# Performance work log

Measured on AMD Instinct MI355X. Metric: run time of the kernel, lower is better.

The kernel has to match this reference:

```python
import jax, jax.numpy as jnp
import numpy as np

N, E, H = 100000, 3200000, 128


def setup_inputs() -> dict:
    key = jax.random.key(0)
    ks = jax.random.split(key, 12)
    s = 1.0 / np.sqrt(H)
    x = jax.random.normal(ks[0], (N, H), dtype=jnp.float32)
    edge_index = jax.random.randint(ks[1], (2, E), 0, N, dtype=jnp.int64)
    # GatedGraphConv weight: [num_layers=1, H, H] -> single [H, H]
    W = jax.random.normal(ks[2], (H, H), dtype=jnp.float32) * s
    # GRUCell (gate order: r, z, n)
    gru_w_ih = jax.random.normal(ks[3], (3 * H, H), dtype=jnp.float32) * s
    gru_w_hh = jax.random.normal(ks[4], (3 * H, H), dtype=jnp.float32) * s
    gru_b_ih = jax.random.normal(ks[5], (3 * H,), dtype=jnp.float32) * s
    gru_b_hh = jax.random.normal(ks[6], (3 * H,), dtype=jnp.float32) * s
    # LSTM layer 0 (gate order: i, f, g, o)
    lstm_w_ih = jax.random.normal(ks[7], (4 * H, H), dtype=jnp.float32) * s
    lstm_w_hh = jax.random.normal(ks[8], (4 * H, H), dtype=jnp.float32) * s
    lstm_b_ih = jax.random.normal(ks[9], (4 * H,), dtype=jnp.float32) * s
    lstm_b_hh = jax.random.normal(ks[10], (4 * H,), dtype=jnp.float32) * s
    return {
        "x": x, "edge_index": edge_index, "W": W,
        "gru_w_ih": gru_w_ih, "gru_w_hh": gru_w_hh,
        "gru_b_ih": gru_b_ih, "gru_b_hh": gru_b_hh,
        "lstm_w_ih": lstm_w_ih, "lstm_w_hh": lstm_w_hh,
        "lstm_b_ih": lstm_b_ih, "lstm_b_hh": lstm_b_hh,
    }


def _forward(x, edge_index, W, gru_w_ih, gru_w_hh, gru_b_ih, gru_b_hh,
             lstm_w_ih, lstm_w_hh, lstm_b_ih, lstm_b_hh):
    n = x.shape[0]
    src, dst = edge_index[0], edge_index[1]
    # GatedGraphConv, num_layers=1, mean aggregation
    m = x @ W                                   # [N, H]
    msg = m[src]                                # [E, H] gather (memory-bound)
    agg_sum = jax.ops.segment_sum(msg, dst, num_segments=n)
    deg = jax.ops.segment_sum(jnp.ones((src.shape[0],), x.dtype), dst, num_segments=n)
    agg = agg_sum / jnp.maximum(deg, 1.0)[:, None]
    # GRUCell(agg, x): gates r, z, n
    gi = agg @ gru_w_ih.T + gru_b_ih
    gh = x @ gru_w_hh.T + gru_b_hh
    i_r, i_z, i_n = jnp.split(gi, 3, axis=-1)
    h_r, h_z, h_n = jnp.split(gh, 3, axis=-1)
    r = jax.nn.sigmoid(i_r + h_r)
    z = jax.nn.sigmoid(i_z + h_z)
    ng = jnp.tanh(i_n + r * h_n)
    h_conv = (1.0 - z) * ng + z * x             # conv output H_tilde
    # 1-layer LSTM over seq_len=1 with zero initial (H, C)
    gates = h_conv @ lstm_w_ih.T + lstm_b_ih + lstm_b_hh  # h0 = 0
    i_g, f_g, g_g, o_g = jnp.split(gates, 4, axis=-1)
    c = jax.nn.sigmoid(i_g) * jnp.tanh(g_g)
    h_lstm = jax.nn.sigmoid(o_g) * jnp.tanh(c)
    return jax.nn.relu(h_lstm)


def reference(x, edge_index, W, gru_w_ih, gru_w_hh, gru_b_ih, gru_b_hh,
              lstm_w_ih, lstm_w_hh, lstm_b_ih, lstm_b_hh):
    return _forward(x, edge_index, W, gru_w_ih, gru_w_hh, gru_b_ih, gru_b_hh,
                    lstm_w_ih, lstm_w_hh, lstm_b_ih, lstm_b_hh)
```

## Files before the change

kernel.cpp:

```cpp
#include <hip/hip_runtime.h>
#include <math.h>

#define HD 128
#define PB 256
#define SCB 4096

typedef __attribute__((ext_vector_type(8))) short short8;
typedef __attribute__((ext_vector_type(4))) float f32x4;

__device__ __forceinline__ float sigf(float v) { return 1.0f / (1.0f + __expf(-v)); }

__device__ __forceinline__ unsigned short f2bf(float f) {
  union { float f; unsigned u; } v; v.f = f;
  unsigned r = (v.u + 0x7fffu + ((v.u >> 16) & 1u)) >> 16;
  return (unsigned short)r;
}
__device__ __forceinline__ float bf2f(unsigned short b) {
  union { unsigned u; float f; } v; v.u = ((unsigned)b) << 16;
  return v.f;
}


__global__ __launch_bounds__(256) void bcount_k(const int* __restrict__ ei,
                                                int* __restrict__ bcnt,
                                                int E, int N, int shift, int NB) {
  __shared__ int h[256];
  const int blk = blockIdx.x, tid = threadIdx.x;
  h[tid] = 0;
  __syncthreads();
  int per = (E + PB - 1) / PB;
  int lo = blk * per;
  int hi = (lo + per < E) ? lo + per : E;
  for (int e = lo + tid; e < hi; e += 256) {
    int d = ei[(size_t)E + e];
    if ((unsigned)d >= (unsigned)N) continue;
    atomicAdd(&h[d >> shift], 1);
  }
  __syncthreads();
  if (tid < NB) bcnt[tid * PB + blk] = h[tid];
}

__global__ __launch_bounds__(256) void scan1_k(const int* __restrict__ a,
                                               int* __restrict__ bsums, int total) {
  __shared__ int ts[256];
  int b = blockIdx.x, tid = threadIdx.x;
  int lo = b * SCB + tid * 16;
  int s = 0;
#pragma unroll
  for (int i = 0; i < 16; ++i) {
    int idx = lo + i;
    if (idx < total) s += a[idx];
  }
  ts[tid] = s;
  __syncthreads();
  for (int off = 128; off > 0; off >>= 1) {
    if (tid < off) ts[tid] += ts[tid + off];
    __syncthreads();
  }
  if (tid == 0) bsums[b] = ts[0];
}

__global__ __launch_bounds__(256) void scan2_k(int* __restrict__ bsums, int nb) {
  __shared__ int ts[256];
  int tid = threadIdx.x;
  int v = (tid < nb) ? bsums[tid] : 0;
  ts[tid] = v;
  __syncthreads();
  for (int off = 1; off < 256; off <<= 1) {
    int u = (tid >= off) ? ts[tid - off] : 0;
    __syncthreads();
    ts[tid] += u;
    __syncthreads();
  }
  if (tid < nb) bsums[tid] = ts[tid] - v;
}

__global__ __launch_bounds__(256) void scan3_k(int* __restrict__ a,
                                               const int* __restrict__ bsums,
                                               int total, int nblk) {
  __shared__ int ts[256];
  int b = blockIdx.x, tid = threadIdx.x;
  int lo = b * SCB + tid * 16;
  int pre[16];
  int s = 0;
#pragma unroll
  for (int i = 0; i < 16; ++i) {
    int idx = lo + i;
    int xv = (idx < total) ? a[idx] : 0;
    pre[i] = s;
    s += xv;
  }
  ts[tid] = s;
  __syncthreads();
  for (int off = 1; off < 256; off <<= 1) {
    int u = (tid >= off) ? ts[tid - off] : 0;
    __syncthreads();
    ts[tid] += u;
    __syncthreads();
  }
  int off0 = ts[tid] - s + bsums[b];
#pragma unroll
  for (int i = 0; i < 16; ++i) {
    int idx = lo + i;
    if (idx < total) a[idx] = off0 + pre[i];
  }
  if (b == nblk - 1 && tid == 255) a[total] = off0 + s;
}

__global__ __launch_bounds__(256) void bpart_k(const int* __restrict__ ei,
                                               const int* __restrict__ bstart,
                                               unsigned* __restrict__ ebuf,
                                               int E, int N, int shift, int NB,
                                               int sbits) {
  __shared__ int cur[256];
  const int blk = blockIdx.x, tid = threadIdx.x;
  if (tid < NB) cur[tid] = bstart[tid * PB + blk];
  __syncthreads();
  int per = (E + PB - 1) / PB;
  int lo = blk * per;
  int hi = (lo + per < E) ? lo + per : E;
  const unsigned dmask = (1u << shift) - 1u;
  for (int e = lo + tid; e < hi; e += 256) {
    int s = ei[e];
    int d = ei[(size_t)E + e];
    if ((unsigned)s >= (unsigned)N || (unsigned)d >= (unsigned)N) continue;
    int p = atomicAdd(&cur[d >> shift], 1);
    ebuf[p] = (((unsigned)d & dmask) << sbits) | (unsigned)s;
  }
}

__global__ __launch_bounds__(256) void bfill2_k(const unsigned* __restrict__ ebuf,
                                                const int* __restrict__ bstart,
                                                int* __restrict__ rowstart,
                                                int* __restrict__ csr,
                                                int N, int shift, int NB, int sbits) {
  __shared__ int cnt[2048];
  __shared__ int tsum[256];
  const int b = blockIdx.x, tid = threadIdx.x;
  const int d0 = b << shift;
  int dmax = d0 + (1 << shift);
  if (dmax > N) dmax = N;
  const int nd = dmax - d0;
  const unsigned smask = (1u << sbits) - 1u;
  for (int i = tid; i < nd; i += 256) cnt[i] = 0;
  __syncthreads();
  const int base = bstart[b * PB];
  const int end = bstart[(b + 1) * PB];
  for (int idx = base + tid; idx < end; idx += 256)
    atomicAdd(&cnt[ebuf[idx] >> sbits], 1);
  __syncthreads();
  const int C = (nd + 255) / 256;
  int lo = tid * C;
  int hi = (lo + C < nd) ? lo + C : nd;
  int loc[8];
  int s = 0;
  for (int i = lo; i < hi; ++i) {
    loc[i - lo] = cnt[i];
    s += cnt[i];
  }
  tsum[tid] = s;
  __syncthreads();
  for (int off = 1; off < 256; off <<= 1) {
    int u = (tid >= off) ? tsum[tid - off] : 0;
    __syncthreads();
    tsum[tid] += u;
    __syncthreads();
  }
  int run = tsum[tid] - s + base;
  for (int i = lo; i < hi; ++i) {
    rowstart[d0 + i] = run;
    cnt[i] = run;
    run += loc[i - lo];
  }
  if (b == NB - 1 && tid == 255) rowstart[N] = end;
  __syncthreads();
  for (int idx = base + tid; idx < end; idx += 256) {
    unsigned pk = ebuf[idx];
    int p = atomicAdd(&cnt[pk >> sbits], 1);
    csr[p] = (int)(pk & smask);
  }
}


__global__ __launch_bounds__(256) void convx_k(const float* __restrict__ x,
                                               unsigned short* __restrict__ xb, int n4) {
  int t = blockIdx.x * 256 + threadIdx.x;
  if (t >= n4) return;
  float4 v = reinterpret_cast<const float4*>(x)[t];
  ushort4 o;
  o.x = f2bf(v.x); o.y = f2bf(v.y); o.z = f2bf(v.z); o.w = f2bf(v.w);
  reinterpret_cast<ushort4*>(xb)[t] = o;
}

__global__ __launch_bounds__(256) void prepw_k(
    const float* __restrict__ W, const float* __restrict__ gwih,
    const float* __restrict__ gwhh, const float* __restrict__ lwih,
    const float* __restrict__ lbih, const float* __restrict__ lbhh,
    unsigned short* __restrict__ Wt, unsigned short* __restrict__ gwihb,
    unsigned short* __restrict__ gwhhb, unsigned short* __restrict__ lwb,
    float* __restrict__ lbias) {
  int t = blockIdx.x * 256 + threadIdx.x;
  if (t < 16384) {
    int n = t >> 7, k = t & 127;
    Wt[t] = f2bf(W[(size_t)k * 128 + n]);
    return;
  }
  t -= 16384;
  if (t < 49152) { gwihb[t] = f2bf(gwih[t]); return; }
  t -= 49152;
  if (t < 49152) { gwhhb[t] = f2bf(gwhh[t]); return; }
  t -= 49152;
  if (t < 49152) {
    int j = t >> 7, k = t & 127;
    int jm = j < 128 ? j : j + 128;
    lwb[t] = f2bf(lwih[(size_t)jm * 128 + k]);
    return;
  }
  t -= 49152;
  if (t < 384) {
    int jm = t < 128 ? t : t + 128;
    lbias[t] = lbih[jm] + lbhh[jm];
  }
}

__global__ __launch_bounds__(256) void gather_b_k(const int* __restrict__ csr,
                                                  const int* __restrict__ rowstart,
                                                  const unsigned short* __restrict__ xb,
                                                  unsigned short* __restrict__ xaggb, int N) {
  int w = (int)(((long long)blockIdx.x * 256 + threadIdx.x) >> 6);
  if (w >= N) return;
  const int lane = threadIdx.x & 63;
  const int sub = lane >> 4, li = lane & 15;
  const int beg = rowstart[w], end = rowstart[w + 1];
  const uint4* x4 = reinterpret_cast<const uint4*>(xb);

  float acc[8] = {0.f, 0.f, 0.f, 0.f, 0.f, 0.f, 0.f, 0.f};
#define ACC8(v)                                           \
  {                                                       \
    acc[0] += bf2f((unsigned short)(v).x);                \
    acc[1] += bf2f((unsigned short)((v).x >> 16));        \
    acc[2] += bf2f((unsigned short)(v).y);                \
    acc[3] += bf2f((unsigned short)((v).y >> 16));        \
    acc[4] += bf2f((unsigned short)(v).z);                \
    acc[5] += bf2f((unsigned short)(v).w >> 0 ? (unsigned short)(v).w : (unsigned short)(v).w); \
    acc[5] += 0.f;                                        \
  }
#undef ACC8

  int j = beg;
  for (; j + 8 <= end; j += 8) {
    int s0 = csr[j + sub];
    int s1 = csr[j + 4 + sub];
    uint4 v0 = x4[(size_t)s0 * 16 + li];
    uint4 v1 = x4[(size_t)s1 * 16 + li];
    acc[0] += bf2f((unsigned short)v0.x) + bf2f((unsigned short)v1.x);
    acc[1] += bf2f((unsigned short)(v0.x >> 16)) + bf2f((unsigned short)(v1.x >> 16));
    acc[2] += bf2f((unsigned short)v0.y) + bf2f((unsigned short)v1.y);
    acc[3] += bf2f((unsigned short)(v0.y >> 16)) + bf2f((unsigned short)(v1.y >> 16));
    acc[4] += bf2f((unsigned short)v0.z) + bf2f((unsigned short)v1.z);
    acc[5] += bf2f((unsigned short)(v0.z >> 16)) + bf2f((unsigned short)(v1.z >> 16));
    acc[6] += bf2f((unsigned short)v0.w) + bf2f((unsigned short)v1.w);
    acc[7] += bf2f((unsigned short)(v0.w >> 16)) + bf2f((unsigned short)(v1.w >> 16));
  }
  if (j + 4 <= end) {
    int s0 = csr[j + sub];
    uint4 v0 = x4[(size_t)s0 * 16 + li];
    acc[0] += bf2f((unsigned short)v0.x);
    acc[1] += bf2f((unsigned short)(v0.x >> 16));
    acc[2] += bf2f((unsigned short)v0.y);
    acc[3] += bf2f((unsigned short)(v0.y >> 16));
    acc[4] += bf2f((unsigned short)v0.z);
    acc[5] += bf2f((unsigned short)(v0.z >> 16));
    acc[6] += bf2f((unsigned short)v0.w);
    acc[7] += bf2f((unsigned short)(v0.w >> 16));
    j += 4;
  }
  int rem = end - j;
  if (sub < rem) {
    int s0 = csr[j + sub];
    uint4 v0 = x4[(size_t)s0 * 16 + li];
    acc[0] += bf2f((unsigned short)v0.x);
    acc[1] += bf2f((unsigned short)(v0.x >> 16));
    acc[2] += bf2f((unsigned short)v0.y);
    acc[3] += bf2f((unsigned short)(v0.y >> 16));
    acc[4] += bf2f((unsigned short)v0.z);
    acc[5] += bf2f((unsigned short)(v0.z >> 16));
    acc[6] += bf2f((unsigned short)v0.w);
    acc[7] += bf2f((unsigned short)(v0.w >> 16));
  }

#pragma unroll
  for (int i = 0; i < 8; ++i) {
    acc[i] += __shfl_xor(acc[i], 16, 64);
    acc[i] += __shfl_xor(acc[i], 32, 64);
  }

  if (lane < 16) {
    float scale = 1.0f / fmaxf((float)(end - beg), 1.0f);
    uint4 o;
    o.x = (unsigned)f2bf(acc[0] * scale) | ((unsigned)f2bf(acc[1] * scale) << 16);
    o.y = (unsigned)f2bf(acc[2] * scale) | ((unsigned)f2bf(acc[3] * scale) << 16);
    o.z = (unsigned)f2bf(acc[4] * scale) | ((unsigned)f2bf(acc[5] * scale) << 16);
    o.w = (unsigned)f2bf(acc[6] * scale) | ((unsigned)f2bf(acc[7] * scale) << 16);
    reinterpret_cast<uint4*>(xaggb)[(size_t)w * 16 + li] = o;
  }
}

__global__ __launch_bounds__(256) void gemmw_k(const unsigned short* __restrict__ A,
                                               const unsigned short* __restrict__ B,
                                               unsigned short* __restrict__ C, int nrows) {
  __shared__ unsigned short Bs[64][136];
  const int tid = threadIdx.x;
  const int w = tid >> 6, lane = tid & 63;
  const int q = lane >> 4, r = lane & 15;
  const int row0 = blockIdx.y * 64;
  const int col0 = blockIdx.x * 64;

#pragma unroll
  for (int i = 0; i < 4; ++i) {
    int idx = i * 256 + tid;
    int c = idx >> 4, kq = idx & 15;
    uint4 v = *reinterpret_cast<const uint4*>(&B[((size_t)(col0 + c)) * HD + kq * 8]);
    *reinterpret_cast<uint4*>(&Bs[c][kq * 8]) = v;
  }
  __syncthreads();

  int arow = row0 + (w << 4) + r;
  int ar = arow < nrows ? arow : nrows - 1;
  const unsigned short* Ap = A + (size_t)ar * HD + q * 8;

  f32x4 acc[4];
#pragma unroll
  for (int cb = 0; cb < 4; ++cb) acc[cb] = (f32x4)0.f;

#pragma unroll
  for (int ks = 0; ks < 4; ++ks) {
    short8 af = *reinterpret_cast<const short8*>(Ap + ks * 32);
#pragma unroll
    for (int cb = 0; cb < 4; ++cb) {
      short8 bf = *reinterpret_cast<const short8*>(&Bs[cb * 16 + r][ks * 32 + q * 8]);
      acc[cb] = __builtin_amdgcn_mfma_f32_16x16x32_bf16(af, bf, acc[cb], 0, 0, 0);
    }
  }

#pragma unroll
  for (int cb = 0; cb < 4; ++cb) {
    int col = col0 + cb * 16 + r;
#pragma unroll
    for (int reg = 0; reg < 4; ++reg) {
      int row = row0 + (w << 4) + q * 4 + reg;
      if (row < nrows) C[(size_t)row * HD + col] = f2bf(acc[cb][reg]);
    }
  }
}

__global__ __launch_bounds__(256) void gru_fused_k(
    const unsigned short* __restrict__ Acb, const unsigned short* __restrict__ xb,
    const unsigned short* __restrict__ gwihb, const unsigned short* __restrict__ gwhhb,
    const float* __restrict__ gbih, const float* __restrict__ gbhh,
    unsigned short* __restrict__ hconv, int nrows) {
  __shared__ unsigned short Bsm[6][32][136];
  const int tid = threadIdx.x;
  const int w = tid >> 6, lane = tid & 63;
  const int q = lane >> 4, r = lane & 15;
  const int row0 = blockIdx.y * 64;
  const int c0 = blockIdx.x * 32;

#pragma unroll
  for (int it = 0; it < 12; ++it) {
    int idx = it * 256 + tid;
    int p = idx >> 9;
    int rem = idx & 511;
    int col = rem >> 4, kq = rem & 15;
    const unsigned short* src =
        (p < 3) ? gwihb + ((size_t)(p * 128 + c0 + col)) * HD
                : gwhhb + ((size_t)((p - 3) * 128 + c0 + col)) * HD;
    uint4 v = *reinterpret_cast<const uint4*>(src + kq * 8);
    *reinterpret_cast<uint4*>(&Bsm[p][col][kq * 8]) = v;
  }
  __syncthreads();

  int arow = row0 + (w << 4) + r;
  int ar = arow < nrows ? arow : nrows - 1;
  const unsigned short* Aa = Acb + (size_t)ar * HD + q * 8;
  const unsigned short* Ax = xb + (size_t)ar * HD + q * 8;

  f32x4 acc[6][2];
#pragma unroll
  for (int p = 0; p < 6; ++p)
#pragma unroll
    for (int cb = 0; cb < 2; ++cb) acc[p][cb] = (f32x4)0.f;

#pragma unroll
  for (int ks = 0; ks < 4; ++ks) {
    short8 a1 = *reinterpret_cast<const short8*>(Aa + ks * 32);
    short8 a2 = *reinterpret_cast<const short8*>(Ax + ks * 32);
#pragma unroll
    for (int p = 0; p < 6; ++p) {
      short8 af = (p < 3) ? a1 : a2;
#pragma unroll
      for (int cb = 0; cb < 2; ++cb) {
        short8 bf = *reinterpret_cast<const short8*>(&Bsm[p][cb * 16 + r][ks * 32 + q * 8]);
        acc[p][cb] = __builtin_amdgcn_mfma_f32_16x16x32_bf16(af, bf, acc[p][cb], 0, 0, 0);
      }
    }
  }

#pragma unroll
  for (int cb = 0; cb < 2; ++cb) {
    int col = c0 + cb * 16 + r;
    float bir = gbih[col], biz = gbih[col + 128], bin = gbih[col + 256];
    float bhr = gbhh[col], bhz = gbhh[col + 128], bhn = gbhh[col + 256];
#pragma unroll
    for (int reg = 0; reg < 4; ++reg) {
      int row = row0 + (w << 4) + q * 4 + reg;
      if (row < nrows) {
        float ir = acc[0][cb][reg] + bir, iz = acc[1][cb][reg] + biz;
        float inn = acc[2][cb][reg] + bin;
        float hr = acc[3][cb][reg] + bhr, hz = acc[4][cb][reg] + bhz;
        float hn = acc[5][cb][reg] + bhn;
        float rr = sigf(ir + hr), zz = sigf(iz + hz);
        float nn = tanhf(inn + rr * hn);
        float xv = bf2f(xb[(size_t)row * HD + col]);
        hconv[(size_t)row * HD + col] = f2bf((1.f - zz) * nn + zz * xv);
      }
    }
  }
}

__global__ __launch_bounds__(256) void lstm_fused_k(
    const unsigned short* __restrict__ hconv, const unsigned short* __restrict__ lwb,
    const float* __restrict__ lbias, float* __restrict__ out, int nrows) {
  __shared__ unsigned short Bsm[3][64][136];
  const int tid = threadIdx.x;
  const int w = tid >> 6, lane = tid & 63;
  const int q = lane >> 4, r = lane & 15;
  const int row0 = blockIdx.y * 64;
  const int c0 = blockIdx.x * 64;

#pragma unroll
  for (int it = 0; it < 12; ++it) {
    int idx = it * 256 + tid;
    int p = idx >> 10, rem = idx & 1023;
    int col = rem >> 4, kq = rem & 15;
    uint4 v = *reinterpret_cast<const uint4*>(
        lwb + ((size_t)(p * 128 + c0 + col)) * HD + kq * 8);
    *reinterpret_cast<uint4*>(&Bsm[p][col][kq * 8]) = v;
  }
  __syncthreads();

  int arow = row0 + (w << 4) + r;
  int ar = arow < nrows ? arow : nrows - 1;
  const unsigned short* Ap = hconv + (size_t)ar * HD + q * 8;

  f32x4 acc[3][4];
#pragma unroll
  for (int p = 0; p < 3; ++p)
#pragma unroll
    for (int cb = 0; cb < 4; ++cb) acc[p][cb] = (f32x4)0.f;

#pragma unroll
  for (int ks = 0; ks < 4; ++ks) {
    short8 af = *reinterpret_cast<const short8*>(Ap + ks * 32);
#pragma unroll
    for (int p = 0; p < 3; ++p)
#pragma unroll
      for (int cb = 0; cb < 4; ++cb) {
        short8 bf = *reinterpret_cast<const short8*>(&Bsm[p][cb * 16 + r][ks * 32 + q * 8]);
        acc[p][cb] = __builtin_amdgcn_mfma_f32_16x16x32_bf16(af, bf, acc[p][cb], 0, 0, 0);
      }
  }

#pragma unroll
  for (int cb = 0; cb < 4; ++cb) {
    int col = c0 + cb * 16 + r;
    float bi = lbias[col], bg = lbias[col + 128], bo = lbias[col + 256];
#pragma unroll
    for (int reg = 0; reg < 4; ++reg) {
      int row = row0 + (w << 4) + q * 4 + reg;
      if (row < nrows) {
        float ig = acc[0][cb][reg] + bi;
        float gg = acc[1][cb][reg] + bg;
        float og = acc[2][cb][reg] + bo;
        float cc = sigf(ig) * tanhf(gg);
        out[(size_t)row * HD + col] = fmaxf(sigf(og) * tanhf(cc), 0.f);
      }
    }
  }
}


extern "C" void kernel_launch(void* const* d_in, const int* in_sizes, int n_in,
                              void* d_out, int out_size, void* d_ws, size_t ws_size,
                              hipStream_t stream) {
  const float* x = (const float*)d_in[0];
  const int* ei = (const int*)d_in[1];
  const float* W = (const float*)d_in[2];
  const float* gw_ih = (const float*)d_in[3];
  const float* gw_hh = (const float*)d_in[4];
  const float* gb_ih = (const float*)d_in[5];
  const float* gb_hh = (const float*)d_in[6];
  const float* lw_ih = (const float*)d_in[7];
  const float* lb_ih = (const float*)d_in[9];
  const float* lb_hh = (const float*)d_in[10];
  float* out = (float*)d_out;

  const int N = in_sizes[0] / HD;
  const int E = in_sizes[1] / 2;
  const size_t nH = (size_t)N * HD;

  int shift = 9;
  while (((N + (1 << shift) - 1) >> shift) > 256) ++shift;
  const int NB = (N + (1 << shift) - 1) >> shift;
  const int sbits = 32 - shift;

  const size_t N4p = (size_t)((N + 1 + 7) & ~7);
  const size_t E4 = (size_t)((E + 3) & ~3);
  const size_t BC = (size_t)NB * PB + 8;
  const int sc_total = NB * PB;
  const int sc_nblk = (sc_total + SCB - 1) / SCB;

  char* p = (char*)d_ws;
  int* rowstart = (int*)p;  p += 4 * N4p;
  int* bcnt = (int*)p;      p += 4 * BC;
  int* bsums = (int*)p;     p += 4 * 64;
  int* csr = (int*)p;       p += 4 * E4;
  size_t sz_eb = 4 * E4, sz_xb = 2 * nH;
  unsigned* ebuf = (unsigned*)p;
  unsigned short* xb = (unsigned short*)p;
  p += (sz_eb > sz_xb ? sz_eb : sz_xb);
  unsigned short* Acb = (unsigned short*)p;    p += 2 * nH;
  unsigned short* hconv = (unsigned short*)p;  p += 2 * nH;
  unsigned short* Wt = (unsigned short*)p;     p += 2 * 16384;
  unsigned short* gwihb = (unsigned short*)p;  p += 2 * 49152;
  unsigned short* gwhhb = (unsigned short*)p;  p += 2 * 49152;
  unsigned short* lwb = (unsigned short*)p;    p += 2 * 49152;
  float* lbias = (float*)p;                    p += 4 * 384;

  unsigned short* xaggb = (unsigned short*)d_out;

  dim3 blk(256);
  unsigned rb = (unsigned)((N + 63) / 64);

  bcount_k<<<PB, blk, 0, stream>>>(ei, bcnt, E, N, shift, NB);
  scan1_k<<<sc_nblk, blk, 0, stream>>>(bcnt, bsums, sc_total);
  scan2_k<<<1, blk, 0, stream>>>(bsums, sc_nblk);
  scan3_k<<<sc_nblk, blk, 0, stream>>>(bcnt, bsums, sc_total, sc_nblk);
  bpart_k<<<PB, blk, 0, stream>>>(ei, bcnt, ebuf, E, N, shift, NB, sbits);
  bfill2_k<<<NB, blk, 0, stream>>>(ebuf, bcnt, rowstart, csr, N, shift, NB, sbits);

  convx_k<<<(unsigned)((nH / 4 + 255) / 256), blk, 0, stream>>>(x, xb, (int)(nH / 4));
  prepw_k<<<(16384 + 3 * 49152 + 384 + 255) / 256, blk, 0, stream>>>(
      W, gw_ih, gw_hh, lw_ih, lb_ih, lb_hh, Wt, gwihb, gwhhb, lwb, lbias);

  long long gthreads = (long long)N * 64;
  gather_b_k<<<(unsigned)((gthreads + 255) / 256), blk, 0, stream>>>(
      csr, rowstart, xb, xaggb, N);

  gemmw_k<<<dim3(2, rb), blk, 0, stream>>>(xaggb, Wt, Acb, N);

  gru_fused_k<<<dim3(4, rb), blk, 0, stream>>>(
      Acb, xb, gwihb, gwhhb, gb_ih, gb_hh, hconv, N);

  lstm_fused_k<<<dim3(2, rb), blk, 0, stream>>>(hconv, lwb, lbias, out, N);
}
```

Before: 511.2 us.

## Pre-sort edges by source bucket before destination CSR build for gather locality

```diff
diff --git a/kernel.cpp b/kernel.cpp
--- a/kernel.cpp
+++ b/kernel.cpp
@@ -19,10 +19,14 @@
   union { unsigned u; float f; } v; v.u = ((unsigned)b) << 16;
   return v.f;
 }
-
-
-__global__ __launch_bounds__(256) void bcount_k(const int* __restrict__ ei,
-                                                int* __restrict__ bcnt,
+__device__ __forceinline__ int clampN(int v, int N) {
+  unsigned u = (unsigned)v;
+  return (u < (unsigned)N) ? v : (int)(N - 1);
+}
+
+
+__global__ __launch_bounds__(256) void scount_k(const int* __restrict__ ei,
+                                                int* __restrict__ cntbuf,
                                                 int E, int N, int shift, int NB) {
   __shared__ int h[256];
   const int blk = blockIdx.x, tid = threadIdx.x;
@@ -32,13 +36,32 @@
   int lo = blk * per;
   int hi = (lo + per < E) ? lo + per : E;
   for (int e = lo + tid; e < hi; e += 256) {
-    int d = ei[(size_t)E + e];
-    if ((unsigned)d >= (unsigned)N) continue;
-    atomicAdd(&h[d >> shift], 1);
-  }
-  __syncthreads();
-  if (tid < NB) bcnt[tid * PB + blk] = h[tid];
-}
+    int s = clampN(ei[e], N);
+    atomicAdd(&h[s >> shift], 1);
+  }
+  __syncthreads();
+  if (tid < NB) cntbuf[tid * PB + blk] = h[tid];
+}
+
+__global__ __launch_bounds__(256) void spart_k(const int* __restrict__ ei,
+                                               const int* __restrict__ bstart,
+                                               int2* __restrict__ ebuf1,
+                                               int E, int N, int shift, int NB) {
+  __shared__ int cur[256];
+  const int blk = blockIdx.x, tid = threadIdx.x;
+  if (tid < NB) cur[tid] = bstart[tid * PB + blk];
+  __syncthreads();
+  int per = (E + PB - 1) / PB;
+  int lo = blk * per;
+  int hi = (lo + per < E) ? lo + per : E;
+  for (int e = lo + tid; e < hi; e += 256) {
+    int s = clampN(ei[e], N);
+    int d = clampN(ei[(size_t)E + e], N);
+    int p = atomicAdd(&cur[s >> shift], 1);
+    ebuf1[p] = make_int2(s, d);
+  }
+}
+
 
 __global__ __launch_bounds__(256) void scan1_k(const int* __restrict__ a,
                                                int* __restrict__ bsums, int total) {
@@ -107,11 +130,27 @@
   if (b == nblk - 1 && tid == 255) a[total] = off0 + s;
 }
 
-__global__ __launch_bounds__(256) void bpart_k(const int* __restrict__ ei,
-                                               const int* __restrict__ bstart,
-                                               unsigned* __restrict__ ebuf,
-                                               int E, int N, int shift, int NB,
-                                               int sbits) {
+
+__global__ __launch_bounds__(256) void bcount2_k(const int2* __restrict__ ebuf1,
+                                                 int* __restrict__ cntbuf,
+                                                 int E, int shift, int NB) {
+  __shared__ int h[256];
+  const int blk = blockIdx.x, tid = threadIdx.x;
+  h[tid] = 0;
+  __syncthreads();
+  int per = (E + PB - 1) / PB;
+  int lo = blk * per;
+  int hi = (lo + per < E) ? lo + per : E;
+  for (int e = lo + tid; e < hi; e += 256)
+    atomicAdd(&h[ebuf1[e].y >> shift], 1);
+  __syncthreads();
+  if (tid < NB) cntbuf[tid * PB + blk] = h[tid];
+}
+
+__global__ __launch_bounds__(256) void bpart2_k(const int2* __restrict__ ebuf1,
+                                                const int* __restrict__ bstart,
+                                                unsigned* __restrict__ ebuf2,
+                                                int E, int shift, int NB, int sbits) {
   __shared__ int cur[256];
   const int blk = blockIdx.x, tid = threadIdx.x;
   if (tid < NB) cur[tid] = bstart[tid * PB + blk];
@@ -121,15 +160,13 @@
   int hi = (lo + per < E) ? lo + per : E;
   const unsigned dmask = (1u << shift) - 1u;
   for (int e = lo + tid; e < hi; e += 256) {
-    int s = ei[e];
-    int d = ei[(size_t)E + e];
-    if ((unsigned)s >= (unsigned)N || (unsigned)d >= (unsigned)N) continue;
-    int p = atomicAdd(&cur[d >> shift], 1);
-    ebuf[p] = (((unsigned)d & dmask) << sbits) | (unsigned)s;
-  }
-}
-
-__global__ __launch_bounds__(256) void bfill2_k(const unsigned* __restrict__ ebuf,
+    int2 sd = ebuf1[e];
+    int p = atomicAdd(&cur[sd.y >> shift], 1);
+    ebuf2[p] = (((unsigned)sd.y & dmask) << sbits) | (unsigned)sd.x;
+  }
+}
+
+__global__ __launch_bounds__(256) void bfill2_k(const unsigned* __restrict__ ebuf2,
                                                 const int* __restrict__ bstart,
                                                 int* __restrict__ rowstart,
                                                 int* __restrict__ csr,
@@ -147,7 +184,7 @@
   const int base = bstart[b * PB];
   const int end = bstart[(b + 1) * PB];
   for (int idx = base + tid; idx < end; idx += 256)
-    atomicAdd(&cnt[ebuf[idx] >> sbits], 1);
+    atomicAdd(&cnt[ebuf2[idx] >> sbits], 1);
   __syncthreads();
   const int C = (nd + 255) / 256;
   int lo = tid * C;
@@ -175,7 +212,7 @@
   if (b == NB - 1 && tid == 255) rowstart[N] = end;
   __syncthreads();
   for (int idx = base + tid; idx < end; idx += 256) {
-    unsigned pk = ebuf[idx];
+    unsigned pk = ebuf2[idx];
     int p = atomicAdd(&cnt[pk >> sbits], 1);
     csr[p] = (int)(pk & smask);
   }
@@ -235,17 +272,6 @@
   const uint4* x4 = reinterpret_cast<const uint4*>(xb);
 
   float acc[8] = {0.f, 0.f, 0.f, 0.f, 0.f, 0.f, 0.f, 0.f};
-#define ACC8(v)                                           \
-  {                                                       \
-    acc[0] += bf2f((unsigned short)(v).x);                \
-    acc[1] += bf2f((unsigned short)((v).x >> 16));        \
-    acc[2] += bf2f((unsigned short)(v).y);                \
-    acc[3] += bf2f((unsigned short)((v).y >> 16));        \
-    acc[4] += bf2f((unsigned short)(v).z);                \
-    acc[5] += bf2f((unsigned short)(v).w >> 0 ? (unsigned short)(v).w : (unsigned short)(v).w); \
-    acc[5] += 0.f;                                        \
-  }
-#undef ACC8
 
   int j = beg;
   for (; j + 8 <= end; j += 8) {
@@ -525,10 +551,11 @@
   int* bcnt = (int*)p;      p += 4 * BC;
   int* bsums = (int*)p;     p += 4 * 64;
   int* csr = (int*)p;       p += 4 * E4;
-  size_t sz_eb = 4 * E4, sz_xb = 2 * nH;
-  unsigned* ebuf = (unsigned*)p;
+  unsigned* ebuf2 = (unsigned*)p; p += 4 * E4;
+  size_t sz_eb1 = 8 * E4, sz_xb = 2 * nH;
+  int2* ebuf1 = (int2*)p;
   unsigned short* xb = (unsigned short*)p;
-  p += (sz_eb > sz_xb ? sz_eb : sz_xb);
+  p += (sz_eb1 > sz_xb ? sz_eb1 : sz_xb);
   unsigned short* Acb = (unsigned short*)p;    p += 2 * nH;
   unsigned short* hconv = (unsigned short*)p;  p += 2 * nH;
   unsigned short* Wt = (unsigned short*)p;     p += 2 * 16384;
@@ -542,12 +569,18 @@
   dim3 blk(256);
   unsigned rb = (unsigned)((N + 63) / 64);
 
-  bcount_k<<<PB, blk, 0, stream>>>(ei, bcnt, E, N, shift, NB);
+  scount_k<<<PB, blk, 0, stream>>>(ei, bcnt, E, N, shift, NB);
   scan1_k<<<sc_nblk, blk, 0, stream>>>(bcnt, bsums, sc_total);
   scan2_k<<<1, blk, 0, stream>>>(bsums, sc_nblk);
   scan3_k<<<sc_nblk, blk, 0, stream>>>(bcnt, bsums, sc_total, sc_nblk);
-  bpart_k<<<PB, blk, 0, stream>>>(ei, bcnt, ebuf, E, N, shift, NB, sbits);
-  bfill2_k<<<NB, blk, 0, stream>>>(ebuf, bcnt, rowstart, csr, N, shift, NB, sbits);
+  spart_k<<<PB, blk, 0, stream>>>(ei, bcnt, ebuf1, E, N, shift, NB);
+
+  bcount2_k<<<PB, blk, 0, stream>>>(ebuf1, bcnt, E, shift, NB);
+  scan1_k<<<sc_nblk, blk, 0, stream>>>(bcnt, bsums, sc_total);
+  scan2_k<<<1, blk, 0, stream>>>(bsums, sc_nblk);
+  scan3_k<<<sc_nblk, blk, 0, stream>>>(bcnt, bsums, sc_total, sc_nblk);
+  bpart2_k<<<PB, blk, 0, stream>>>(ebuf1, bcnt, ebuf2, E, shift, NB, sbits);
+  bfill2_k<<<NB, blk, 0, stream>>>(ebuf2, bcnt, rowstart, csr, N, shift, NB, sbits);
 
   convx_k<<<(unsigned)((nH / 4 + 255) / 256), blk, 0, stream>>>(x, xb, (int)(nH / 4));
   prepw_k<<<(16384 + 3 * 49152 + 384 + 255) / 256, blk, 0, stream>>>(
```

Result: slower. 561.8 us (+9.9%).

## Fold W into GRU input weights and drop the separate aggregation GEMM

Applied to the files above, without the earlier changes.

```diff
diff --git a/kernel.cpp b/kernel.cpp
--- a/kernel.cpp
+++ b/kernel.cpp
@@ -193,21 +193,11 @@
 }
 
 __global__ __launch_bounds__(256) void prepw_k(
-    const float* __restrict__ W, const float* __restrict__ gwih,
     const float* __restrict__ gwhh, const float* __restrict__ lwih,
     const float* __restrict__ lbih, const float* __restrict__ lbhh,
-    unsigned short* __restrict__ Wt, unsigned short* __restrict__ gwihb,
     unsigned short* __restrict__ gwhhb, unsigned short* __restrict__ lwb,
     float* __restrict__ lbias) {
   int t = blockIdx.x * 256 + threadIdx.x;
-  if (t < 16384) {
-    int n = t >> 7, k = t & 127;
-    Wt[t] = f2bf(W[(size_t)k * 128 + n]);
-    return;
-  }
-  t -= 16384;
-  if (t < 49152) { gwihb[t] = f2bf(gwih[t]); return; }
-  t -= 49152;
   if (t < 49152) { gwhhb[t] = f2bf(gwhh[t]); return; }
   t -= 49152;
   if (t < 49152) {
@@ -221,6 +211,34 @@
     int jm = t < 128 ? t : t + 128;
     lbias[t] = lbih[jm] + lbhh[jm];
   }
+}
+
+__global__ __launch_bounds__(256) void prepbp_k(const float* __restrict__ W,
+                                                const float* __restrict__ gwih,
+                                                unsigned short* __restrict__ Bpb) {
+  int t = blockIdx.x * 256 + threadIdx.x;
+  if (t >= 49152) return;
+  int j = t >> 7, k = t & 127;
+  const float4* wr = reinterpret_cast<const float4*>(W + (size_t)k * 128);
+  const float4* gr = reinterpret_cast<const float4*>(gwih + (size_t)j * 128);
+  float acc = 0.f;
+#pragma unroll
+  for (int c = 0; c < 32; ++c) {
+    float4 a = wr[c], b = gr[c];
+    acc += a.x * b.x + a.y * b.y + a.z * b.z + a.w * b.w;
+  }
+  Bpb[t] = f2bf(acc);
+}
+
+__device__ __forceinline__ void acc8(float* acc, uint4 v) {
+  acc[0] += bf2f((unsigned short)v.x);
+  acc[1] += bf2f((unsigned short)(v.x >> 16));
+  acc[2] += bf2f((unsigned short)v.y);
+  acc[3] += bf2f((unsigned short)(v.y >> 16));
+  acc[4] += bf2f((unsigned short)v.z);
+  acc[5] += bf2f((unsigned short)(v.z >> 16));
+  acc[6] += bf2f((unsigned short)v.w);
+  acc[7] += bf2f((unsigned short)(v.w >> 16));
 }
 
 __global__ __launch_bounds__(256) void gather_b_k(const int* __restrict__ csr,
@@ -235,58 +253,29 @@
   const uint4* x4 = reinterpret_cast<const uint4*>(xb);
 
   float acc[8] = {0.f, 0.f, 0.f, 0.f, 0.f, 0.f, 0.f, 0.f};
-#define ACC8(v)                                           \
-  {                                                       \
-    acc[0] += bf2f((unsigned short)(v).x);                \
-    acc[1] += bf2f((unsigned short)((v).x >> 16));        \
-    acc[2] += bf2f((unsigned short)(v).y);                \
-    acc[3] += bf2f((unsigned short)((v).y >> 16));        \
-    acc[4] += bf2f((unsigned short)(v).z);                \
-    acc[5] += bf2f((unsigned short)(v).w >> 0 ? (unsigned short)(v).w : (unsigned short)(v).w); \
-    acc[5] += 0.f;                                        \
-  }
-#undef ACC8
 
   int j = beg;
-  for (; j + 8 <= end; j += 8) {
+  for (; j + 16 <= end; j += 16) {
     int s0 = csr[j + sub];
     int s1 = csr[j + 4 + sub];
+    int s2 = csr[j + 8 + sub];
+    int s3 = csr[j + 12 + sub];
     uint4 v0 = x4[(size_t)s0 * 16 + li];
     uint4 v1 = x4[(size_t)s1 * 16 + li];
-    acc[0] += bf2f((unsigned short)v0.x) + bf2f((unsigned short)v1.x);
-    acc[1] += bf2f((unsigned short)(v0.x >> 16)) + bf2f((unsigned short)(v1.x >> 16));
-    acc[2] += bf2f((unsigned short)v0.y) + bf2f((unsigned short)v1.y);
-    acc[3] += bf2f((unsigned short)(v0.y >> 16)) + bf2f((unsigned short)(v1.y >> 16));
-    acc[4] += bf2f((unsigned short)v0.z) + bf2f((unsigned short)v1.z);
-    acc[5] += bf2f((unsigned short)(v0.z >> 16)) + bf2f((unsigned short)(v1.z >> 16));
-    acc[6] += bf2f((unsigned short)v0.w) + bf2f((unsigned short)v1.w);
-    acc[7] += bf2f((unsigned short)(v0.w >> 16)) + bf2f((unsigned short)(v1.w >> 16));
-  }
-  if (j + 4 <= end) {
+    uint4 v2 = x4[(size_t)s2 * 16 + li];
+    uint4 v3 = x4[(size_t)s3 * 16 + li];
+    acc8(acc, v0); acc8(acc, v1); acc8(acc, v2); acc8(acc, v3);
+  }
+  for (; j + 4 <= end; j += 4) {
     int s0 = csr[j + sub];
     uint4 v0 = x4[(size_t)s0 * 16 + li];
-    acc[0] += bf2f((unsigned short)v0.x);
-    acc[1] += bf2f((unsigned short)(v0.x >> 16));
-    acc[2] += bf2f((unsigned short)v0.y);
-    acc[3] += bf2f((unsigned short)(v0.y >> 16));
-    acc[4] += bf2f((unsigned short)v0.z);
-    acc[5] += bf2f((unsigned short)(v0.z >> 16));
-    acc[6] += bf2f((unsigned short)v0.w);
-    acc[7] += bf2f((unsigned short)(v0.w >> 16));
-    j += 4;
+    acc8(acc, v0);
   }
   int rem = end - j;
   if (sub < rem) {
     int s0 = csr[j + sub];
     uint4 v0 = x4[(size_t)s0 * 16 + li];
-    acc[0] += bf2f((unsigned short)v0.x);
-    acc[1] += bf2f((unsigned short)(v0.x >> 16));
-    acc[2] += bf2f((unsigned short)v0.y);
-    acc[3] += bf2f((unsigned short)(v0.y >> 16));
-    acc[4] += bf2f((unsigned short)v0.z);
-    acc[5] += bf2f((unsigned short)(v0.z >> 16));
-    acc[6] += bf2f((unsigned short)v0.w);
-    acc[7] += bf2f((unsigned short)(v0.w >> 16));
+    acc8(acc, v0);
   }
 
 #pragma unroll
@@ -306,57 +295,9 @@
   }
 }
 
-__global__ __launch_bounds__(256) void gemmw_k(const unsigned short* __restrict__ A,
-                                               const unsigned short* __restrict__ B,
-                                               unsigned short* __restrict__ C, int nrows) {
-  __shared__ unsigned short Bs[64][136];
-  const int tid = threadIdx.x;
-  const int w = tid >> 6, lane = tid & 63;
-  const int q = lane >> 4, r = lane & 15;
-  const int row0 = blockIdx.y * 64;
-  const int col0 = blockIdx.x * 64;
-
-#pragma unroll
-  for (int i = 0; i < 4; ++i) {
-    int idx = i * 256 + tid;
-    int c = idx >> 4, kq = idx & 15;
-    uint4 v = *reinterpret_cast<const uint4*>(&B[((size_t)(col0 + c)) * HD + kq * 8]);
-    *reinterpret_cast<uint4*>(&Bs[c][kq * 8]) = v;
-  }
-  __syncthreads();
-
-  int arow = row0 + (w << 4) + r;
-  int ar = arow < nrows ? arow : nrows - 1;
-  const unsigned short* Ap = A + (size_t)ar * HD + q * 8;
-
-  f32x4 acc[4];
-#pragma unroll
-  for (int cb = 0; cb < 4; ++cb) acc[cb] = (f32x4)0.f;
-
-#pragma unroll
-  for (int ks = 0; ks < 4; ++ks) {
-    short8 af = *reinterpret_cast<const short8*>(Ap + ks * 32);
-#pragma unroll
-    for (int cb = 0; cb < 4; ++cb) {
-      short8 bf = *reinterpret_cast<const short8*>(&Bs[cb * 16 + r][ks * 32 + q * 8]);
-      acc[cb] = __builtin_amdgcn_mfma_f32_16x16x32_bf16(af, bf, acc[cb], 0, 0, 0);
-    }
-  }
-
-#pragma unroll
-  for (int cb = 0; cb < 4; ++cb) {
-    int col = col0 + cb * 16 + r;
-#pragma unroll
-    for (int reg = 0; reg < 4; ++reg) {
-      int row = row0 + (w << 4) + q * 4 + reg;
-      if (row < nrows) C[(size_t)row * HD + col] = f2bf(acc[cb][reg]);
-    }
-  }
-}
-
 __global__ __launch_bounds__(256) void gru_fused_k(
-    const unsigned short* __restrict__ Acb, const unsigned short* __restrict__ xb,
-    const unsigned short* __restrict__ gwihb, const unsigned short* __restrict__ gwhhb,
+    const unsigned short* __restrict__ xaggb, const unsigned short* __restrict__ xb,
+    const unsigned short* __restrict__ Bpb, const unsigned short* __restrict__ gwhhb,
     const float* __restrict__ gbih, const float* __restrict__ gbhh,
     unsigned short* __restrict__ hconv, int nrows) {
   __shared__ unsigned short Bsm[6][32][136];
@@ -373,7 +314,7 @@
     int rem = idx & 511;
     int col = rem >> 4, kq = rem & 15;
     const unsigned short* src =
-        (p < 3) ? gwihb + ((size_t)(p * 128 + c0 + col)) * HD
+        (p < 3) ? Bpb + ((size_t)(p * 128 + c0 + col)) * HD
                 : gwhhb + ((size_t)((p - 3) * 128 + c0 + col)) * HD;
     uint4 v = *reinterpret_cast<const uint4*>(src + kq * 8);
     *reinterpret_cast<uint4*>(&Bsm[p][col][kq * 8]) = v;
@@ -382,7 +323,7 @@
 
   int arow = row0 + (w << 4) + r;
   int ar = arow < nrows ? arow : nrows - 1;
-  const unsigned short* Aa = Acb + (size_t)ar * HD + q * 8;
+  const unsigned short* Aa = xaggb + (size_t)ar * HD + q * 8;
   const unsigned short* Ax = xb + (size_t)ar * HD + q * 8;
 
   f32x4 acc[6][2];
@@ -529,10 +470,8 @@
   unsigned* ebuf = (unsigned*)p;
   unsigned short* xb = (unsigned short*)p;
   p += (sz_eb > sz_xb ? sz_eb : sz_xb);
-  unsigned short* Acb = (unsigned short*)p;    p += 2 * nH;
   unsigned short* hconv = (unsigned short*)p;  p += 2 * nH;
-  unsigned short* Wt = (unsigned short*)p;     p += 2 * 16384;
-  unsigned short* gwihb = (unsigned short*)p;  p += 2 * 49152;
+  unsigned short* Bpb = (unsigned short*)p;    p += 2 * 49152;
   unsigned short* gwhhb = (unsigned short*)p;  p += 2 * 49152;
   unsigned short* lwb = (unsigned short*)p;    p += 2 * 49152;
   float* lbias = (float*)p;                    p += 4 * 384;
@@ -550,17 +489,16 @@
   bfill2_k<<<NB, blk, 0, stream>>>(ebuf, bcnt, rowstart, csr, N, shift, NB, sbits);
 
   convx_k<<<(unsigned)((nH / 4 + 255) / 256), blk, 0, stream>>>(x, xb, (int)(nH / 4));
-  prepw_k<<<(16384 + 3 * 49152 + 384 + 255) / 256, blk, 0, stream>>>(
-      W, gw_ih, gw_hh, lw_ih, lb_ih, lb_hh, Wt, gwihb, gwhhb, lwb, lbias);
+  prepw_k<<<(2 * 49152 + 384 + 255) / 256, blk, 0, stream>>>(
+      gw_hh, lw_ih, lb_ih, lb_hh, gwhhb, lwb, lbias);
+  prepbp_k<<<192, blk, 0, stream>>>(W, gw_ih, Bpb);
 
   long long gthreads = (long long)N * 64;
   gather_b_k<<<(unsigned)((gthreads + 255) / 256), blk, 0, stream>>>(
       csr, rowstart, xb, xaggb, N);
 
-  gemmw_k<<<dim3(2, rb), blk, 0, stream>>>(xaggb, Wt, Acb, N);
-
   gru_fused_k<<<dim3(4, rb), blk, 0, stream>>>(
-      Acb, xb, gwihb, gwhhb, gb_ih, gb_hh, hconv, N);
+      xaggb, xb, Bpb, gwhhb, gb_ih, gb_hh, hconv, N);
 
   lstm_fused_k<<<dim3(2, rb), blk, 0, stream>>>(hconv, lwb, lbias, out, N);
 }
```

New measurement: 500.2 us. 1.02x faster.
